# Performance work log

Hardware: AMD Instinct MI355X
Metric: run time of the kernel (lower is better)

## Reference

```python
import jax, jax.numpy as jnp
import numpy as np
from jax import lax

EPS_BN = 1e-5
EPS_NORM = 1e-12
MEM_CHUNK = 8192


def _conv(x, w, b):
    # x: [B,C,H,W], w: [O,I,3,3], stride 2, pad 1 (torch Conv2d semantics)
    y = lax.conv_general_dilated(x, w, window_strides=(2, 2),
                                 padding=((1, 1), (1, 1)),
                                 dimension_numbers=("NCHW", "OIHW", "NCHW"))
    return y + b[None, :, None, None]


def _bn(x, gamma, beta, mean, var):
    # eval-mode BatchNorm2d with running statistics
    inv = lax.rsqrt(var + EPS_BN)
    return (x - mean[None, :, None, None]) * (gamma * inv)[None, :, None, None] + beta[None, :, None, None]


def setup_inputs() -> dict:
    key = jax.random.key(0)
    ks = jax.random.split(key, 20)
    B, H = 256, 64
    N_MEM, D = 262144, 64
    inp = {
        "x": jax.random.normal(ks[0], (B, 1, H, H), dtype=jnp.float32),
        "memory_bank": jax.random.normal(ks[1], (N_MEM, D), dtype=jnp.float32),
    }
    specs = [(1, 16), (16, 32), (32, 64)]
    for i, (cin, cout) in enumerate(specs):
        fan_in = cin * 9
        bound = 1.0 / np.sqrt(fan_in)
        inp[f"w{i}"] = jax.random.uniform(ks[2 + 6 * i], (cout, cin, 3, 3), jnp.float32, -bound, bound)
        inp[f"b{i}"] = jax.random.uniform(ks[3 + 6 * i], (cout,), jnp.float32, -bound, bound)
        inp[f"gamma{i}"] = jnp.ones((cout,), jnp.float32)
        inp[f"beta{i}"] = jnp.zeros((cout,), jnp.float32)
        inp[f"mean{i}"] = 0.1 * jax.random.normal(ks[4 + 6 * i], (cout,), jnp.float32)
        inp[f"var{i}"] = jax.random.uniform(ks[5 + 6 * i], (cout,), jnp.float32, 0.5, 1.5)
    return inp


def _forward(x, memory_bank,
             w0, b0, gamma0, beta0, mean0, var0,
             w1, b1, gamma1, beta1, mean1, var1,
             w2, b2, gamma2, beta2, mean2, var2):
    B = x.shape[0]
    D = 64
    # backbone: (conv -> bn -> relu) x3, stride 2 each -> H/8
    h = x
    params = [(w0, b0, gamma0, beta0, mean0, var0),
              (w1, b1, gamma1, beta1, mean1, var1),
              (w2, b2, gamma2, beta2, mean2, var2)]
    for (w, b, g, bt, m, v) in params:
        h = jax.nn.relu(_bn(_conv(h, w, b), g, bt, m, v))
    # [B,64,8,8] -> [B,P,64], L2 normalize
    emb = h.transpose(0, 2, 3, 1).reshape(B, -1, D)
    emb = emb / jnp.clip(jnp.linalg.norm(emb, axis=-1, keepdims=True), EPS_NORM)
    P = emb.shape[1]
    q = emb.reshape(-1, D)                      # [Q, D]
    q_sq = jnp.sum(q * q, axis=-1)              # [Q]
    # memory bank is L2-normalized at set_memory_bank time
    mb = memory_bank / jnp.clip(jnp.linalg.norm(memory_bank, axis=-1, keepdims=True), EPS_NORM)
    n_chunks = mb.shape[0] // MEM_CHUNK
    mb_chunks = mb.reshape(n_chunks, MEM_CHUNK, D)

    def body(best, mc):
        # blockwise squared L2 via gram trick, online running min (never full matrix)
        d2 = q_sq[:, None] + jnp.sum(mc * mc, axis=-1)[None, :] - 2.0 * (q @ mc.T)
        d = jnp.sqrt(jnp.clip(d2, 0.0))
        return jnp.minimum(best, jnp.min(d, axis=1)), None

    best, _ = lax.scan(body, jnp.full((q.shape[0],), jnp.inf, q.dtype), mb_chunks)
    patch_dist = best.reshape(B, P)
    return jnp.max(patch_dist, axis=1)          # reduction='max'


def reference(x, memory_bank,
              w0, b0, gamma0, beta0, mean0, var0,
              w1, b1, gamma1, beta1, mean1, var1,
              w2, b2, gamma2, beta2, mean2, var2):
    return _forward(x, memory_bank,
                    w0, b0, gamma0, beta0, mean0, var0,
                    w1, b1, gamma1, beta1, mean1, var1,
                    w2, b2, gamma2, beta2, mean2, var2)
```

## Files before the change

kernel.cpp:

```cpp
#include <hip/hip_runtime.h>
#include <math.h>

typedef __bf16 v8bf __attribute__((ext_vector_type(8)));
typedef __bf16 v4bf __attribute__((ext_vector_type(4)));
typedef float  v16f __attribute__((ext_vector_type(16)));
typedef float  v4f  __attribute__((ext_vector_type(4)));

#define EPS_BN 1e-5f
#define Q_TOTAL 16384
#define N_MEM   262144
#define SLICES  16
#define SLICE_LEN (N_MEM / SLICES)
#define CHUNK   256
#define NCHUNKS (SLICE_LEN / CHUNK)

__device__ __forceinline__ void gload_lds16(const void* g, void* l) {
    __builtin_amdgcn_global_load_lds(
        (const __attribute__((address_space(1))) void*)g,
        (__attribute__((address_space(3))) void*)l, 16, 0, 0);
}

__global__ void conv0_kernel(const float* __restrict__ x,
                             const float* __restrict__ w, const float* __restrict__ bias,
                             const float* __restrict__ gamma, const float* __restrict__ beta,
                             const float* __restrict__ mean, const float* __restrict__ var,
                             float* __restrict__ out) {
    int idx = blockIdx.x * 256 + threadIdx.x;
    int xo = idx & 31, yo = (idx >> 5) & 31, c = (idx >> 10) & 15, b = idx >> 14;
    const float* xp = x + (size_t)b * 4096;
    const float* wc = w + c * 9;
    float acc = 0.f;
#pragma unroll
    for (int dy = 0; dy < 3; ++dy) {
        int iy = 2 * yo + dy - 1;
        if (iy < 0) continue;
#pragma unroll
        for (int dx = 0; dx < 3; ++dx) {
            int ix = 2 * xo + dx - 1;
            if (ix < 0) continue;
            acc += wc[dy * 3 + dx] * xp[iy * 64 + ix];
        }
    }
    acc += bias[c];
    float sc = gamma[c] * rsqrtf(var[c] + EPS_BN);
    float v  = (acc - mean[c]) * sc + beta[c];
    out[idx] = fmaxf(v, 0.f);
}

__global__ void conv1_kernel(const float* __restrict__ in,
                             const float* __restrict__ w, const float* __restrict__ bias,
                             const float* __restrict__ gamma, const float* __restrict__ beta,
                             const float* __restrict__ mean, const float* __restrict__ var,
                             float* __restrict__ out) {
    __shared__ float in_s[16384];
    __shared__ float w_s[1152];
    __shared__ float sc_s[8], sh_s[8];
    int b = blockIdx.x >> 2, cg = blockIdx.x & 3;
    int t = threadIdx.x;
    const float4* ip4 = (const float4*)(in + (size_t)b * 16384);
    float4* is4 = (float4*)in_s;
    for (int i = t; i < 4096; i += 256) is4[i] = ip4[i];
    for (int i = t; i < 1152; i += 256) w_s[i] = w[cg * 1152 + i];
    if (t < 8) {
        int c = cg * 8 + t;
        float sc = gamma[c] * rsqrtf(var[c] + EPS_BN);
        sc_s[t] = sc;
        sh_s[t] = (bias[c] - mean[c]) * sc + beta[c];
    }
    __syncthreads();
    int xo = t & 15, yo = t >> 4;
    float acc[8];
#pragma unroll
    for (int c = 0; c < 8; ++c) acc[c] = 0.f;
    int iy0 = 2 * yo - 1, ix0 = 2 * xo - 1;
    for (int ci = 0; ci < 16; ++ci) {
        const float* base = in_s + ci * 1024;
        float r[9];
#pragma unroll
        for (int dy = 0; dy < 3; ++dy) {
            int iy = iy0 + dy;
            int iyc = iy < 0 ? 0 : iy;
#pragma unroll
            for (int dx = 0; dx < 3; ++dx) {
                int ix = ix0 + dx;
                int ixc = ix < 0 ? 0 : ix;
                float v = base[iyc * 32 + ixc];
                r[dy * 3 + dx] = (iy >= 0 && ix >= 0) ? v : 0.f;
            }
        }
#pragma unroll
        for (int c = 0; c < 8; ++c) {
            const float* wp = w_s + (c * 16 + ci) * 9;
#pragma unroll
            for (int k = 0; k < 9; ++k) acc[c] = fmaf(wp[k], r[k], acc[c]);
        }
    }
#pragma unroll
    for (int c = 0; c < 8; ++c) {
        float v = fmaf(acc[c], sc_s[c], sh_s[c]);
        out[((size_t)(b * 32 + cg * 8 + c) * 16 + yo) * 16 + xo] = fmaxf(v, 0.f);
    }
}

__global__ void conv2_kernel(const float* __restrict__ in,
                             const float* __restrict__ w, const float* __restrict__ bias,
                             const float* __restrict__ gamma, const float* __restrict__ beta,
                             const float* __restrict__ mean, const float* __restrict__ var,
                             float* __restrict__ out) {
    __shared__ float in_s[8192];
    __shared__ float w_s[4608];
    __shared__ float sc_s[16], sh_s[16];
    int b = blockIdx.x >> 2, cg = blockIdx.x & 3;
    int t = threadIdx.x;
    const float4* ip4 = (const float4*)(in + (size_t)b * 8192);
    float4* is4 = (float4*)in_s;
    for (int i = t; i < 2048; i += 256) is4[i] = ip4[i];
    for (int i = t; i < 4608; i += 256) w_s[i] = w[cg * 4608 + i];
    if (t < 16) {
        int c = cg * 16 + t;
        float sc = gamma[c] * rsqrtf(var[c] + EPS_BN);
        sc_s[t] = sc;
        sh_s[t] = (bias[c] - mean[c]) * sc + beta[c];
    }
    __syncthreads();
    int xo = t & 7, yo = (t >> 3) & 7, cs = t >> 6;
    float acc[4];
#pragma unroll
    for (int l = 0; l < 4; ++l) acc[l] = 0.f;
    int iy0 = 2 * yo - 1, ix0 = 2 * xo - 1;
    for (int ci = 0; ci < 32; ++ci) {
        const float* base = in_s + ci * 256;
        float r[9];
#pragma unroll
        for (int dy = 0; dy < 3; ++dy) {
            int iy = iy0 + dy;
            int iyc = iy < 0 ? 0 : iy;
#pragma unroll
            for (int dx = 0; dx < 3; ++dx) {
                int ix = ix0 + dx;
                int ixc = ix < 0 ? 0 : ix;
                float v = base[iyc * 16 + ixc];
                r[dy * 3 + dx] = (iy >= 0 && ix >= 0) ? v : 0.f;
            }
        }
#pragma unroll
        for (int l = 0; l < 4; ++l) {
            const float* wp = w_s + ((cs * 4 + l) * 32 + ci) * 9;
#pragma unroll
            for (int k = 0; k < 9; ++k) acc[l] = fmaf(wp[k], r[k], acc[l]);
        }
    }
#pragma unroll
    for (int l = 0; l < 4; ++l) {
        int c = cg * 16 + cs * 4 + l;
        float v = fmaf(acc[l], sc_s[cs * 4 + l], sh_s[cs * 4 + l]);
        out[((size_t)(b * 64 + c) * 8 + yo) * 8 + xo] = fmaxf(v, 0.f);
    }
}

__global__ void qnorm_kernel(const float* __restrict__ y2,
                             __bf16* __restrict__ q, float* __restrict__ qsq,
                             unsigned int* __restrict__ mind2) {
    __shared__ float  L1s[4096];
    __shared__ __bf16 L2s[4096];
    int b = blockIdx.x, t = threadIdx.x;
    mind2[b * 64 + t] = 0x7f800000u;
    const float* src = y2 + (size_t)b * 4096;
    for (int i = t; i < 4096; i += 64) L1s[i] = src[i];
    __syncthreads();
    int p = t;
    float ss = 0.f;
    for (int d = 0; d < 64; ++d) { float v = L1s[d * 64 + p]; ss += v * v; }
    float inv = 1.f / fmaxf(sqrtf(ss), 1e-12f);
    float q2 = 0.f;
    for (int d = 0; d < 64; ++d) {
        float v = L1s[d * 64 + p] * inv;
        __bf16 bv = (__bf16)v;
        L2s[p * 64 + d] = bv;
        float fb = (float)bv;
        q2 += fb * fb;
    }
    qsq[b * 64 + p] = q2;
    __syncthreads();
    for (int p2 = 0; p2 < 64; ++p2)
        q[((size_t)(b * 64 + p2)) * 64 + t] = L2s[p2 * 64 + t];
}

__global__ void mbnorm_kernel(const float* __restrict__ mb,
                              __bf16* __restrict__ mbbf) {
    int tid = blockIdx.x * 256 + threadIdx.x;
    int row = tid >> 4, sub = tid & 15;
    const float4 v = *(const float4*)(mb + (size_t)row * 64 + sub * 4);
    float ss = v.x * v.x + v.y * v.y + v.z * v.z + v.w * v.w;
#pragma unroll
    for (int o = 1; o < 16; o <<= 1) ss += __shfl_xor(ss, o, 64);
    float inv = 1.f / fmaxf(sqrtf(ss), 1e-12f);
    v4bf o;
    o[0] = (__bf16)(v.x * inv);
    o[1] = (__bf16)(v.y * inv);
    o[2] = (__bf16)(v.z * inv);
    o[3] = (__bf16)(v.w * inv);
    *(v4bf*)(mbbf + (size_t)row * 64 + sub * 4) = o;
}

__global__ __launch_bounds__(256)
void dist_kernel(const __bf16* __restrict__ q, const float* __restrict__ qsq,
                 const __bf16* __restrict__ mb,
                 unsigned int* __restrict__ mind2) {
    __shared__ __align__(16) __bf16 Bs[2][CHUNK * 64];
    const int t = threadIdx.x;
    const int wave = t >> 6, lane = t & 63;
    const int n32 = lane & 31, half = lane >> 5;
    const int mbase = blockIdx.x * 256 + wave * 64;
    const int slice = blockIdx.y;

    v8bf a[2][4];
#pragma unroll
    for (int s = 0; s < 2; ++s)
#pragma unroll
        for (int ks = 0; ks < 4; ++ks)
            a[s][ks] = *(const v8bf*)(q + (size_t)(mbase + s * 32 + n32) * 64
                                        + ks * 16 + half * 8);

    float tmax[2][16];
#pragma unroll
    for (int s = 0; s < 2; ++s)
#pragma unroll
        for (int r = 0; r < 16; ++r) tmax[s][r] = -3.0e38f;

    v16f Z;
#pragma unroll
    for (int r = 0; r < 16; ++r) Z[r] = 0.f;

    const int r0 = t >> 3, c0 = (t & 7) ^ (r0 & 7);
    const __bf16* gp = mb + (size_t)slice * SLICE_LEN * 64 + r0 * 64 + c0 * 8;
    const int wbase = wave * 1024;

#pragma unroll
    for (int j = 0; j < 8; ++j) {
        gload_lds16(gp, (char*)Bs[0] + j * 4096 + wbase);
        gp += 2048;
    }

    const int sw = (n32 & 7) << 4;
    int offk[4];
#pragma unroll
    for (int ks = 0; ks < 4; ++ks) offk[ks] = (((ks * 2 + half) << 4) ^ sw);

    auto step = [&](const char* bp, char* pdst, bool more) {
        __syncthreads();
        if (more) {
#pragma unroll
            for (int j = 0; j < 8; ++j) {
                gload_lds16(gp, pdst + j * 4096 + wbase);
                gp += 2048;
            }
        }
        const char* tp = bp + n32 * 128;
        v8bf be[4], bo[4];
#pragma unroll
        for (int ks = 0; ks < 4; ++ks) {
            be[ks] = *(const v8bf*)(tp + offk[ks]);
            bo[ks] = *(const v8bf*)(tp + 4096 + offk[ks]);
        }
#pragma unroll 1
        for (int p = 0; p < 4; ++p) {
            v16f A0 = __builtin_amdgcn_mfma_f32_32x32x16_bf16(a[0][0], be[0], Z, 0, 0, 0);
            v16f A1 = __builtin_amdgcn_mfma_f32_32x32x16_bf16(a[1][0], be[0], Z, 0, 0, 0);
#pragma unroll
            for (int ks = 1; ks < 4; ++ks) {
                A0 = __builtin_amdgcn_mfma_f32_32x32x16_bf16(a[0][ks], be[ks], A0, 0, 0, 0);
                A1 = __builtin_amdgcn_mfma_f32_32x32x16_bf16(a[1][ks], be[ks], A1, 0, 0, 0);
            }
            v16f B0 = __builtin_amdgcn_mfma_f32_32x32x16_bf16(a[0][0], bo[0], Z, 0, 0, 0);
            v16f B1 = __builtin_amdgcn_mfma_f32_32x32x16_bf16(a[1][0], bo[0], Z, 0, 0, 0);
#pragma unroll
            for (int ks = 1; ks < 4; ++ks) {
                B0 = __builtin_amdgcn_mfma_f32_32x32x16_bf16(a[0][ks], bo[ks], B0, 0, 0, 0);
                B1 = __builtin_amdgcn_mfma_f32_32x32x16_bf16(a[1][ks], bo[ks], B1, 0, 0, 0);
            }
            if (p < 3) {
                const char* tn = tp + (p + 1) * 8192;
#pragma unroll
                for (int ks = 0; ks < 4; ++ks) {
                    be[ks] = *(const v8bf*)(tn + offk[ks]);
                    bo[ks] = *(const v8bf*)(tn + 4096 + offk[ks]);
                }
            }
#pragma unroll
            for (int r = 0; r < 16; ++r) {
                tmax[0][r] = fmaxf(fmaxf(A0[r], B0[r]), tmax[0][r]);
                tmax[1][r] = fmaxf(fmaxf(A1[r], B1[r]), tmax[1][r]);
            }
        }
    };

    for (int ch = 0; ch < NCHUNKS; ch += 2) {
        step((const char*)Bs[0], (char*)Bs[1], ch + 1 < NCHUNKS);
        step((const char*)Bs[1], (char*)Bs[0], ch + 2 < NCHUNKS);
    }

#pragma unroll
    for (int s = 0; s < 2; ++s)
#pragma unroll
        for (int r = 0; r < 16; ++r) {
            float v = tmax[s][r];
            v = fmaxf(v, __shfl_xor(v, 1, 64));
            v = fmaxf(v, __shfl_xor(v, 2, 64));
            v = fmaxf(v, __shfl_xor(v, 4, 64));
            v = fmaxf(v, __shfl_xor(v, 8, 64));
            v = fmaxf(v, __shfl_xor(v, 16, 64));
            tmax[s][r] = v;
        }
    if (n32 == 0) {
#pragma unroll
        for (int s = 0; s < 2; ++s)
#pragma unroll
            for (int r = 0; r < 16; ++r) {
                int row = (r & 3) + 8 * (r >> 2) + 4 * half;
                int m = mbase + s * 32 + row;
                float dd = fmaxf(qsq[m] + 1.0f - 2.0f * tmax[s][r], 0.f);
                atomicMin(mind2 + m, __float_as_uint(dd));
            }
    }
}

__global__ void finalize_kernel(const unsigned int* __restrict__ mind2,
                                float* __restrict__ out) {
    int b = blockIdx.x, l = threadIdx.x;
    float v = __uint_as_float(mind2[b * 64 + l]);
    float d = sqrtf(fmaxf(v, 0.f));
#pragma unroll
    for (int o = 1; o < 64; o <<= 1) d = fmaxf(d, __shfl_xor(d, o, 64));
    if (l == 0) out[b] = d;
}

extern "C" void kernel_launch(void* const* d_in, const int* in_sizes, int n_in,
                              void* d_out, int out_size, void* d_ws, size_t ws_size,
                              hipStream_t stream) {
    (void)in_sizes; (void)n_in; (void)out_size; (void)ws_size;
    const float* x     = (const float*)d_in[0];
    const float* mbank = (const float*)d_in[1];
    const float* w0 = (const float*)d_in[2],  *b0 = (const float*)d_in[3];
    const float* g0 = (const float*)d_in[4],  *be0 = (const float*)d_in[5];
    const float* mn0 = (const float*)d_in[6], *vr0 = (const float*)d_in[7];
    const float* w1 = (const float*)d_in[8],  *b1 = (const float*)d_in[9];
    const float* g1 = (const float*)d_in[10], *be1 = (const float*)d_in[11];
    const float* mn1 = (const float*)d_in[12], *vr1 = (const float*)d_in[13];
    const float* w2 = (const float*)d_in[14], *b2 = (const float*)d_in[15];
    const float* g2 = (const float*)d_in[16], *be2 = (const float*)d_in[17];
    const float* mn2 = (const float*)d_in[18], *vr2 = (const float*)d_in[19];

    char* ws = (char*)d_ws;
    float*        y0    = (float*)(ws + 0);
    float*        y1    = (float*)(ws + 16777216);
    float*        y2    = (float*)(ws + 25165824);
    __bf16*       qbf   = (__bf16*)(ws + 29360128);
    float*        qsq   = (float*)(ws + 31457280);
    __bf16*       mbbf  = (__bf16*)(ws + 31522816);
    unsigned int* mind2 = (unsigned int*)(ws + 66125824);

    conv0_kernel<<<16384, 256, 0, stream>>>(x, w0, b0, g0, be0, mn0, vr0, y0);
    conv1_kernel<<<1024, 256, 0, stream>>>(y0, w1, b1, g1, be1, mn1, vr1, y1);
    conv2_kernel<<<1024, 256, 0, stream>>>(y1, w2, b2, g2, be2, mn2, vr2, y2);
    qnorm_kernel<<<256, 64, 0, stream>>>(y2, qbf, qsq, mind2);
    mbnorm_kernel<<<16384, 256, 0, stream>>>(mbank, mbbf);
    dist_kernel<<<dim3(64, SLICES), 256, 0, stream>>>(qbf, qsq, mbbf, mind2);
    finalize_kernel<<<256, 64, 0, stream>>>(mind2, (float*)d_out);
}
```

Baseline: 672.2 us.

## Switch distance GEMM to 16x16x32 MFMA tiles with smaller LDS chunks

```diff
diff --git a/kernel.cpp b/kernel.cpp
--- a/kernel.cpp
+++ b/kernel.cpp
@@ -11,7 +11,7 @@
 #define N_MEM   262144
 #define SLICES  16
 #define SLICE_LEN (N_MEM / SLICES)
-#define CHUNK   256
+#define CHUNK   128
 #define NCHUNKS (SLICE_LEN / CHUNK)
 
 __device__ __forceinline__ void gload_lds16(const void* g, void* l) {
@@ -203,95 +203,95 @@
     *(v4bf*)(mbbf + (size_t)row * 64 + sub * 4) = o;
 }
 
-__global__ __launch_bounds__(256)
+__global__ __launch_bounds__(256, 4)
 void dist_kernel(const __bf16* __restrict__ q, const float* __restrict__ qsq,
                  const __bf16* __restrict__ mb,
                  unsigned int* __restrict__ mind2) {
     __shared__ __align__(16) __bf16 Bs[2][CHUNK * 64];
     const int t = threadIdx.x;
     const int wave = t >> 6, lane = t & 63;
-    const int n32 = lane & 31, half = lane >> 5;
+    const int c16 = lane & 15;
+    const int kblk = lane >> 4;
     const int mbase = blockIdx.x * 256 + wave * 64;
     const int slice = blockIdx.y;
 
-    v8bf a[2][4];
-#pragma unroll
-    for (int s = 0; s < 2; ++s)
-#pragma unroll
-        for (int ks = 0; ks < 4; ++ks)
-            a[s][ks] = *(const v8bf*)(q + (size_t)(mbase + s * 32 + n32) * 64
-                                        + ks * 16 + half * 8);
-
-    float tmax[2][16];
-#pragma unroll
-    for (int s = 0; s < 2; ++s)
-#pragma unroll
-        for (int r = 0; r < 16; ++r) tmax[s][r] = -3.0e38f;
-
-    v16f Z;
-#pragma unroll
-    for (int r = 0; r < 16; ++r) Z[r] = 0.f;
+    v8bf a[4][2];
+#pragma unroll
+    for (int s = 0; s < 4; ++s)
+#pragma unroll
+        for (int ks = 0; ks < 2; ++ks)
+            a[s][ks] = *(const v8bf*)(q + (size_t)(mbase + s * 16 + c16) * 64
+                                        + ks * 32 + kblk * 8);
+
+    float tmax[4][4];
+#pragma unroll
+    for (int s = 0; s < 4; ++s)
+#pragma unroll
+        for (int r = 0; r < 4; ++r) tmax[s][r] = -3.0e38f;
+
+    v4f Z;
+#pragma unroll
+    for (int r = 0; r < 4; ++r) Z[r] = 0.f;
 
     const int r0 = t >> 3, c0 = (t & 7) ^ (r0 & 7);
     const __bf16* gp = mb + (size_t)slice * SLICE_LEN * 64 + r0 * 64 + c0 * 8;
     const int wbase = wave * 1024;
 
 #pragma unroll
-    for (int j = 0; j < 8; ++j) {
+    for (int j = 0; j < 4; ++j) {
         gload_lds16(gp, (char*)Bs[0] + j * 4096 + wbase);
         gp += 2048;
     }
 
-    const int sw = (n32 & 7) << 4;
-    int offk[4];
-#pragma unroll
-    for (int ks = 0; ks < 4; ++ks) offk[ks] = (((ks * 2 + half) << 4) ^ sw);
+    const int rowb = c16 * 128;
+    int offk[2];
+#pragma unroll
+    for (int ks = 0; ks < 2; ++ks) offk[ks] = (((kblk + 4 * ks) ^ (lane & 7)) << 4);
 
     auto step = [&](const char* bp, char* pdst, bool more) {
         __syncthreads();
         if (more) {
 #pragma unroll
-            for (int j = 0; j < 8; ++j) {
+            for (int j = 0; j < 4; ++j) {
                 gload_lds16(gp, pdst + j * 4096 + wbase);
                 gp += 2048;
             }
         }
-        const char* tp = bp + n32 * 128;
-        v8bf be[4], bo[4];
-#pragma unroll
-        for (int ks = 0; ks < 4; ++ks) {
+        const char* tp = bp + rowb;
+        v8bf be[2], bo[2];
+#pragma unroll
+        for (int ks = 0; ks < 2; ++ks) {
             be[ks] = *(const v8bf*)(tp + offk[ks]);
-            bo[ks] = *(const v8bf*)(tp + 4096 + offk[ks]);
+            bo[ks] = *(const v8bf*)(tp + 2048 + offk[ks]);
         }
 #pragma unroll 1
         for (int p = 0; p < 4; ++p) {
-            v16f A0 = __builtin_amdgcn_mfma_f32_32x32x16_bf16(a[0][0], be[0], Z, 0, 0, 0);
-            v16f A1 = __builtin_amdgcn_mfma_f32_32x32x16_bf16(a[1][0], be[0], Z, 0, 0, 0);
-#pragma unroll
-            for (int ks = 1; ks < 4; ++ks) {
-                A0 = __builtin_amdgcn_mfma_f32_32x32x16_bf16(a[0][ks], be[ks], A0, 0, 0, 0);
-                A1 = __builtin_amdgcn_mfma_f32_32x32x16_bf16(a[1][ks], be[ks], A1, 0, 0, 0);
-            }
-            v16f B0 = __builtin_amdgcn_mfma_f32_32x32x16_bf16(a[0][0], bo[0], Z, 0, 0, 0);
-            v16f B1 = __builtin_amdgcn_mfma_f32_32x32x16_bf16(a[1][0], bo[0], Z, 0, 0, 0);
-#pragma unroll
-            for (int ks = 1; ks < 4; ++ks) {
-                B0 = __builtin_amdgcn_mfma_f32_32x32x16_bf16(a[0][ks], bo[ks], B0, 0, 0, 0);
-                B1 = __builtin_amdgcn_mfma_f32_32x32x16_bf16(a[1][ks], bo[ks], B1, 0, 0, 0);
-            }
+            v4f Ae[4], Ao[4];
+#pragma unroll
+            for (int s = 0; s < 4; ++s)
+                Ae[s] = __builtin_amdgcn_mfma_f32_16x16x32_bf16(a[s][0], be[0], Z, 0, 0, 0);
+#pragma unroll
+            for (int s = 0; s < 4; ++s)
+                Ao[s] = __builtin_amdgcn_mfma_f32_16x16x32_bf16(a[s][0], bo[0], Z, 0, 0, 0);
+#pragma unroll
+            for (int s = 0; s < 4; ++s)
+                Ae[s] = __builtin_amdgcn_mfma_f32_16x16x32_bf16(a[s][1], be[1], Ae[s], 0, 0, 0);
+#pragma unroll
+            for (int s = 0; s < 4; ++s)
+                Ao[s] = __builtin_amdgcn_mfma_f32_16x16x32_bf16(a[s][1], bo[1], Ao[s], 0, 0, 0);
             if (p < 3) {
-                const char* tn = tp + (p + 1) * 8192;
-#pragma unroll
-                for (int ks = 0; ks < 4; ++ks) {
+                const char* tn = tp + (p + 1) * 4096;
+#pragma unroll
+                for (int ks = 0; ks < 2; ++ks) {
                     be[ks] = *(const v8bf*)(tn + offk[ks]);
-                    bo[ks] = *(const v8bf*)(tn + 4096 + offk[ks]);
+                    bo[ks] = *(const v8bf*)(tn + 2048 + offk[ks]);
                 }
             }
 #pragma unroll
-            for (int r = 0; r < 16; ++r) {
-                tmax[0][r] = fmaxf(fmaxf(A0[r], B0[r]), tmax[0][r]);
-                tmax[1][r] = fmaxf(fmaxf(A1[r], B1[r]), tmax[1][r]);
-            }
+            for (int s = 0; s < 4; ++s)
+#pragma unroll
+                for (int r = 0; r < 4; ++r)
+                    tmax[s][r] = fmaxf(fmaxf(Ae[s][r], Ao[s][r]), tmax[s][r]);
         }
     };
 
@@ -301,24 +301,22 @@
     }
 
 #pragma unroll
-    for (int s = 0; s < 2; ++s)
-#pragma unroll
-        for (int r = 0; r < 16; ++r) {
+    for (int s = 0; s < 4; ++s)
+#pragma unroll
+        for (int r = 0; r < 4; ++r) {
             float v = tmax[s][r];
             v = fmaxf(v, __shfl_xor(v, 1, 64));
             v = fmaxf(v, __shfl_xor(v, 2, 64));
             v = fmaxf(v, __shfl_xor(v, 4, 64));
             v = fmaxf(v, __shfl_xor(v, 8, 64));
-            v = fmaxf(v, __shfl_xor(v, 16, 64));
             tmax[s][r] = v;
         }
-    if (n32 == 0) {
-#pragma unroll
-        for (int s = 0; s < 2; ++s)
-#pragma unroll
-            for (int r = 0; r < 16; ++r) {
-                int row = (r & 3) + 8 * (r >> 2) + 4 * half;
-                int m = mbase + s * 32 + row;
+    if (c16 == 0) {
+#pragma unroll
+        for (int s = 0; s < 4; ++s)
+#pragma unroll
+            for (int r = 0; r < 4; ++r) {
+                int m = mbase + s * 16 + kblk * 4 + r;
                 float dd = fmaxf(qsq[m] + 1.0f - 2.0f * tmax[s][r], 0.f);
                 atomicMin(mind2 + m, __float_as_uint(dd));
             }
```

Result: faster. 587.4 us (-12.6%).
